# Optimization experiments

Measured on AMD Instinct MI355X. Metric: run time of the kernel, lower is better.

Reference implementation:

```python
import jax, jax.numpy as jnp
import numpy as np

MAX_NODE = 20
SEG = [100, 20, 3200, 160, 400, 20, 400]  # split sizes, total 4300

_DIMS = {"h1": (5, 16), "h2": (16, 8), "h3": (8, 8),
         "f1": (8, 16), "f2": (16, 8), "f3": (8, 8),
         "d1": (13, 16), "d2": (16, 8), "d3": (8, 8),
         "g1": (8, 16), "g2": (16, 8), "g3": (8, 8),
         "fc1": (29, 32), "fc2": (32, 16), "fc3": (16, 8), "fc4": (8, 1)}


def _mk(key, shape):
    return jax.random.normal(key, shape, dtype=jnp.float32) * 0.1


def setup_inputs() -> dict:
    key = jax.random.key(0)
    ks = jax.random.split(key, 8 + 2 * len(_DIMS))
    # assemble the flat [1,4300] input: node feats, masks/adjacency summaries
    ni = jax.random.normal(ks[0], (100,), dtype=jnp.float32)
    valid = jax.random.bernoulli(ks[1], 0.8, (20,)).astype(jnp.float32)
    gmats = jax.random.uniform(ks[2], (3200,), dtype=jnp.float32)
    gmasks = jax.random.bernoulli(ks[3], 0.5, (160,)).astype(jnp.float32)
    summ = jax.random.bernoulli(ks[4], 0.3, (400,)).astype(jnp.float32)
    running = jax.random.bernoulli(ks[5], 0.5, (20,)).astype(jnp.float32)
    backmap = jax.random.bernoulli(ks[6], 0.3, (400,)).astype(jnp.float32)
    inp = jnp.concatenate([ni, valid, gmats, gmasks, summ, running, backmap])[None, :]
    out = {"input": inp}
    i = 8
    for name, (din, dout) in _DIMS.items():
        out[name + "_w"] = _mk(ks[i], (din, dout)); i += 1
        out[name + "_b"] = _mk(ks[i], (dout,)); i += 1
    return out


def reference(input, h1_w, h1_b, h2_w, h2_b, h3_w, h3_b,
              f1_w, f1_b, f2_w, f2_b, f3_w, f3_b,
              d1_w, d1_b, d2_w, d2_b, d3_w, d3_b,
              g1_w, g1_b, g2_w, g2_b, g3_w, g3_b,
              fc1_w, fc1_b, fc2_w, fc2_b, fc3_w, fc3_b, fc4_w, fc4_b):
    relu = jax.nn.relu
    gl = lambda x, w, b: x @ w + b
    x0 = input[0]
    ni = x0[:100].reshape(MAX_NODE, 5)
    valid = x0[100:120].reshape(1, 1, MAX_NODE)
    # x0[120:3320] = gcn_mats (split in original but never used)
    summ = x0[3480:3880].reshape(1, MAX_NODE, MAX_NODE)
    running = x0[3880:3900].reshape(1, 1, MAX_NODE)
    backmap = x0[3900:4300].reshape(1, MAX_NODE, MAX_NODE)
    # original overwrites every gcn_mask with zeros(20,1)
    zmask = jnp.zeros((MAX_NODE, 1), dtype=input.dtype)

    def fblock(y):
        for w, b in ((f1_w, f1_b), (f2_w, f2_b), (f3_w, f3_b),
                     (f1_w, f1_b), (f2_w, f2_b), (f3_w, f3_b)):
            y = relu(gl(y, w, b))
        return y

    x = relu(gl(ni, h1_w, h1_b))
    x = relu(gl(x, h2_w, h2_b))
    x = relu(gl(x, h3_w, h3_b))  # (20, 8)
    y = x
    for blk in range(8):
        src = y if blk == 5 else x  # block 5 forgets to reset y = x (as in source)
        y = fblock(src) * zmask
        x = x + y
    gcn_output = x  # (20, 8)

    xc = jnp.concatenate([ni, gcn_output], axis=1)  # (20, 13)
    s = relu(gl(xc, d1_w, d1_b))
    s = relu(gl(s, d2_w, d2_b))
    s = relu(gl(s, d3_w, d3_b))
    s = jnp.matmul(summ, s)  # (1, 20, 8)
    dag_summary = s
    s = relu(gl(s, g1_w, g1_b))
    s = relu(gl(s, g2_w, g2_b))
    s = relu(gl(s, g3_w, g3_b))
    global_summary = jnp.matmul(running, s)  # (1, 1, 8)
    dag_ext = jnp.matmul(backmap, dag_summary)  # (1, 20, 8)
    glob_ext = jnp.tile(global_summary, (1, MAX_NODE, 1))  # (1, 20, 8)

    merge = jnp.concatenate([ni[None], gcn_output[None], dag_ext, glob_ext], axis=2)  # (1,20,29)
    y2 = relu(gl(merge, fc1_w, fc1_b))
    y2 = relu(gl(y2, fc2_w, fc2_b))
    y2 = relu(gl(y2, fc3_w, fc3_b))
    logits = gl(y2, fc4_w, fc4_b).reshape(1, 1, MAX_NODE)
    logits = logits + (valid - 1.0) * 10000.0
    return jax.nn.softmax(logits, axis=-1).reshape(1, MAX_NODE)
```

## Files before the change

kernel.cpp:

```cpp
#include <hip/hip_runtime.h>
#include <math.h>

#define NT 256

#define CP(dst, src, n) do { for (int i = tid; i < (n); i += NT) (dst)[i] = (src)[i]; } while (0)

template<int DIN, int DOUT, bool RELU>
__device__ __forceinline__ void dense20(int tid, const float* __restrict__ in,
                                        const float* __restrict__ w,
                                        const float* __restrict__ bi,
                                        float* __restrict__ out) {
    constexpr int N = 20 * DOUT;
    #pragma unroll
    for (int i0 = 0; i0 < N; i0 += NT) {
        int i = i0 + tid;
        if (i < N) {
            int r = i / DOUT, c = i % DOUT;
            float acc = bi[c];
            #pragma unroll
            for (int k = 0; k < DIN; ++k)
                acc = fmaf(in[r * DIN + k], w[k * DOUT + c], acc);
            out[i] = RELU ? fmaxf(acc, 0.0f) : acc;
        }
    }
}

__global__ __launch_bounds__(NT)
void fused_net_kernel(const float* __restrict__ inp,
                      const float* __restrict__ h1w, const float* __restrict__ h1b,
                      const float* __restrict__ h2w, const float* __restrict__ h2b,
                      const float* __restrict__ h3w, const float* __restrict__ h3b,
                      const float* __restrict__ d1w, const float* __restrict__ d1b,
                      const float* __restrict__ d2w, const float* __restrict__ d2b,
                      const float* __restrict__ d3w, const float* __restrict__ d3b,
                      const float* __restrict__ g1w, const float* __restrict__ g1b,
                      const float* __restrict__ g2w, const float* __restrict__ g2b,
                      const float* __restrict__ g3w, const float* __restrict__ g3b,
                      const float* __restrict__ fc1w, const float* __restrict__ fc1b,
                      const float* __restrict__ fc2w, const float* __restrict__ fc2b,
                      const float* __restrict__ fc3w, const float* __restrict__ fc3b,
                      const float* __restrict__ fc4w, const float* __restrict__ fc4b,
                      float* __restrict__ out) {
    const int tid = threadIdx.x;

    __shared__ float s_ni[100];
    __shared__ float s_valid[20];
    __shared__ float s_summ[400];
    __shared__ float s_run[20];
    __shared__ float s_back[400];
    __shared__ float s_h1w[80],  s_h1b[16];
    __shared__ float s_h2w[128], s_h2b[8];
    __shared__ float s_h3w[64],  s_h3b[8];
    __shared__ float s_d1w[208], s_d1b[16];
    __shared__ float s_d2w[128], s_d2b[8];
    __shared__ float s_d3w[64],  s_d3b[8];
    __shared__ float s_g1w[128], s_g1b[16];
    __shared__ float s_g2w[128], s_g2b[8];
    __shared__ float s_g3w[64],  s_g3b[8];
    __shared__ float s_fc1w[928], s_fc1b[32];
    __shared__ float s_fc2w[512], s_fc2b[16];
    __shared__ float s_fc3w[128], s_fc3b[8];
    __shared__ float s_fc4w[8],   s_fc4b[1];
    __shared__ float s_bufA[640];
    __shared__ float s_bufB[640];
    __shared__ float s_gcn[160];
    __shared__ float s_dag[160];
    __shared__ float s_glob[8];
    __shared__ float s_logit[20];

    CP(s_ni,    inp,        100);
    CP(s_valid, inp + 100,  20);
    CP(s_summ,  inp + 3480, 400);
    CP(s_run,   inp + 3880, 20);
    CP(s_back,  inp + 3900, 400);
    CP(s_h1w, h1w, 80);   CP(s_h1b, h1b, 16);
    CP(s_h2w, h2w, 128);  CP(s_h2b, h2b, 8);
    CP(s_h3w, h3w, 64);   CP(s_h3b, h3b, 8);
    CP(s_d1w, d1w, 208);  CP(s_d1b, d1b, 16);
    CP(s_d2w, d2w, 128);  CP(s_d2b, d2b, 8);
    CP(s_d3w, d3w, 64);   CP(s_d3b, d3b, 8);
    CP(s_g1w, g1w, 128);  CP(s_g1b, g1b, 16);
    CP(s_g2w, g2w, 128);  CP(s_g2b, g2b, 8);
    CP(s_g3w, g3w, 64);   CP(s_g3b, g3b, 8);
    CP(s_fc1w, fc1w, 928); CP(s_fc1b, fc1b, 32);
    CP(s_fc2w, fc2w, 512); CP(s_fc2b, fc2b, 16);
    CP(s_fc3w, fc3w, 128); CP(s_fc3b, fc3b, 8);
    CP(s_fc4w, fc4w, 8);   CP(s_fc4b, fc4b, 1);
    __syncthreads();

    dense20<5, 16, true>(tid, s_ni,   s_h1w, s_h1b, s_bufA); __syncthreads();
    dense20<16, 8, true>(tid, s_bufA, s_h2w, s_h2b, s_bufB); __syncthreads();
    dense20<8,  8, true>(tid, s_bufB, s_h3w, s_h3b, s_gcn);  __syncthreads();

    {
        int i = tid;
        if (i < 320) {
            int r = i >> 4, c = i & 15;
            float acc = s_d1b[c];
            #pragma unroll
            for (int k = 0; k < 5; ++k)
                acc = fmaf(s_ni[r * 5 + k], s_d1w[k * 16 + c], acc);
            #pragma unroll
            for (int k = 0; k < 8; ++k)
                acc = fmaf(s_gcn[r * 8 + k], s_d1w[(5 + k) * 16 + c], acc);
            s_bufA[i] = fmaxf(acc, 0.0f);
        }
        int j = tid + NT;
        if (j < 320) {
            int r = j >> 4, c = j & 15;
            float acc = s_d1b[c];
            #pragma unroll
            for (int k = 0; k < 5; ++k)
                acc = fmaf(s_ni[r * 5 + k], s_d1w[k * 16 + c], acc);
            #pragma unroll
            for (int k = 0; k < 8; ++k)
                acc = fmaf(s_gcn[r * 8 + k], s_d1w[(5 + k) * 16 + c], acc);
            s_bufA[j] = fmaxf(acc, 0.0f);
        }
    }
    __syncthreads();
    dense20<16, 8, true>(tid, s_bufA, s_d2w, s_d2b, s_bufB); __syncthreads();
    dense20<8,  8, true>(tid, s_bufB, s_d3w, s_d3b, s_bufA); __syncthreads();

    if (tid < 160) {
        int r = tid >> 3, c = tid & 7;
        float acc = 0.0f;
        #pragma unroll
        for (int k = 0; k < 20; ++k)
            acc = fmaf(s_summ[r * 20 + k], s_bufA[k * 8 + c], acc);
        s_dag[tid] = acc;
    }
    __syncthreads();

    dense20<8, 16, true>(tid, s_dag,  s_g1w, s_g1b, s_bufA); __syncthreads();
    dense20<16, 8, true>(tid, s_bufA, s_g2w, s_g2b, s_bufB); __syncthreads();
    dense20<8,  8, true>(tid, s_bufB, s_g3w, s_g3b, s_bufA); __syncthreads();

    if (tid < 160) {
        int r = tid >> 3, c = tid & 7;
        float acc = 0.0f;
        #pragma unroll
        for (int k = 0; k < 20; ++k)
            acc = fmaf(s_back[r * 20 + k], s_dag[k * 8 + c], acc);
        s_bufB[tid] = acc;
    } else if (tid < 168) {
        int c = tid - 160;
        float acc = 0.0f;
        #pragma unroll
        for (int k = 0; k < 20; ++k)
            acc = fmaf(s_run[k], s_bufA[k * 8 + c], acc);
        s_glob[c] = acc;
    }
    __syncthreads();

    #pragma unroll
    for (int i0 = 0; i0 < 640; i0 += NT) {
        int i = i0 + tid;
        if (i < 640) {
            int r = i >> 5, c = i & 31;
            float acc = s_fc1b[c];
            #pragma unroll
            for (int k = 0; k < 5; ++k)
                acc = fmaf(s_ni[r * 5 + k], s_fc1w[k * 32 + c], acc);
            #pragma unroll
            for (int k = 0; k < 8; ++k)
                acc = fmaf(s_gcn[r * 8 + k], s_fc1w[(5 + k) * 32 + c], acc);
            #pragma unroll
            for (int k = 0; k < 8; ++k)
                acc = fmaf(s_bufB[r * 8 + k], s_fc1w[(13 + k) * 32 + c], acc);
            #pragma unroll
            for (int k = 0; k < 8; ++k)
                acc = fmaf(s_glob[k], s_fc1w[(21 + k) * 32 + c], acc);
            s_bufA[i] = fmaxf(acc, 0.0f);
        }
    }
    __syncthreads();
    dense20<32, 16, true>(tid, s_bufA, s_fc2w, s_fc2b, s_bufB); __syncthreads();
    dense20<16, 8, true>(tid, s_bufB, s_fc3w, s_fc3b, s_dag);   __syncthreads();

    if (tid < 20) {
        float acc = s_fc4b[0];
        #pragma unroll
        for (int k = 0; k < 8; ++k)
            acc = fmaf(s_dag[tid * 8 + k], s_fc4w[k], acc);
        s_logit[tid] = acc + (s_valid[tid] - 1.0f) * 10000.0f;
    }
    __syncthreads();

    if (tid == 0) {
        float m = s_logit[0];
        #pragma unroll
        for (int r = 1; r < 20; ++r) m = fmaxf(m, s_logit[r]);
        float e[20];
        float sum = 0.0f;
        #pragma unroll
        for (int r = 0; r < 20; ++r) { e[r] = __expf(s_logit[r] - m); sum += e[r]; }
        float inv = 1.0f / sum;
        #pragma unroll
        for (int r = 0; r < 20; ++r) out[r] = e[r] * inv;
    }
}

extern "C" void kernel_launch(void* const* d_in, const int* in_sizes, int n_in,
                              void* d_out, int out_size, void* d_ws, size_t ws_size,
                              hipStream_t stream) {
    const float* inp = (const float*)d_in[0];
    const float* h1w = (const float*)d_in[1];  const float* h1b = (const float*)d_in[2];
    const float* h2w = (const float*)d_in[3];  const float* h2b = (const float*)d_in[4];
    const float* h3w = (const float*)d_in[5];  const float* h3b = (const float*)d_in[6];
    const float* d1w = (const float*)d_in[13]; const float* d1b = (const float*)d_in[14];
    const float* d2w = (const float*)d_in[15]; const float* d2b = (const float*)d_in[16];
    const float* d3w = (const float*)d_in[17]; const float* d3b = (const float*)d_in[18];
    const float* g1w = (const float*)d_in[19]; const float* g1b = (const float*)d_in[20];
    const float* g2w = (const float*)d_in[21]; const float* g2b = (const float*)d_in[22];
    const float* g3w = (const float*)d_in[23]; const float* g3b = (const float*)d_in[24];
    const float* fc1w = (const float*)d_in[25]; const float* fc1b = (const float*)d_in[26];
    const float* fc2w = (const float*)d_in[27]; const float* fc2b = (const float*)d_in[28];
    const float* fc3w = (const float*)d_in[29]; const float* fc3b = (const float*)d_in[30];
    const float* fc4w = (const float*)d_in[31]; const float* fc4b = (const float*)d_in[32];
    float* out = (float*)d_out;

    fused_net_kernel<<<1, NT, 0, stream>>>(inp,
        h1w, h1b, h2w, h2b, h3w, h3b,
        d1w, d1b, d2w, d2b, d3w, d3b,
        g1w, g1b, g2w, g2b, g3w, g3b,
        fc1w, fc1b, fc2w, fc2b, fc3w, fc3b, fc4w, fc4b,
        out);
}
```

Measured before the change: 125.3 us.

## Shrink block to one wavefront, vectorize shared loads, parallelize softmax output

Reduces the block from 256 to 64 threads, one wave64 wavefront, so barriers become cheap and stages loop over outputs with unrolled strides. Global-to-shared copies use float4 loads with 16-byte-aligned shared arrays. The final softmax is spread across 20 threads that each write one output instead of one thread writing all 20. Each thread now does more serial work per layer, which trades parallel compute for lower synchronisation cost.

```diff
diff --git a/kernel.cpp b/kernel.cpp
--- a/kernel.cpp
+++ b/kernel.cpp
@@ -1,9 +1,11 @@
 #include <hip/hip_runtime.h>
 #include <math.h>
 
-#define NT 256
-
-#define CP(dst, src, n) do { for (int i = tid; i < (n); i += NT) (dst)[i] = (src)[i]; } while (0)
+#define NT 64
+
+#define CP4(dst, src, n) do { \
+    const float4* _s4 = (const float4*)(src); float4* _d4 = (float4*)(dst); \
+    for (int i = tid; i < (n) / 4; i += NT) _d4[i] = _s4[i]; } while (0)
 
 template<int DIN, int DOUT, bool RELU>
 __device__ __forceinline__ void dense20(int tid, const float* __restrict__ in,
@@ -43,92 +45,85 @@
                       float* __restrict__ out) {
     const int tid = threadIdx.x;
 
-    __shared__ float s_ni[100];
-    __shared__ float s_valid[20];
-    __shared__ float s_summ[400];
-    __shared__ float s_run[20];
-    __shared__ float s_back[400];
-    __shared__ float s_h1w[80],  s_h1b[16];
-    __shared__ float s_h2w[128], s_h2b[8];
-    __shared__ float s_h3w[64],  s_h3b[8];
-    __shared__ float s_d1w[208], s_d1b[16];
-    __shared__ float s_d2w[128], s_d2b[8];
-    __shared__ float s_d3w[64],  s_d3b[8];
-    __shared__ float s_g1w[128], s_g1b[16];
-    __shared__ float s_g2w[128], s_g2b[8];
-    __shared__ float s_g3w[64],  s_g3b[8];
-    __shared__ float s_fc1w[928], s_fc1b[32];
-    __shared__ float s_fc2w[512], s_fc2b[16];
-    __shared__ float s_fc3w[128], s_fc3b[8];
-    __shared__ float s_fc4w[8],   s_fc4b[1];
-    __shared__ float s_bufA[640];
-    __shared__ float s_bufB[640];
-    __shared__ float s_gcn[160];
-    __shared__ float s_dag[160];
-    __shared__ float s_glob[8];
-    __shared__ float s_logit[20];
-
-    CP(s_ni,    inp,        100);
-    CP(s_valid, inp + 100,  20);
-    CP(s_summ,  inp + 3480, 400);
-    CP(s_run,   inp + 3880, 20);
-    CP(s_back,  inp + 3900, 400);
-    CP(s_h1w, h1w, 80);   CP(s_h1b, h1b, 16);
-    CP(s_h2w, h2w, 128);  CP(s_h2b, h2b, 8);
-    CP(s_h3w, h3w, 64);   CP(s_h3b, h3b, 8);
-    CP(s_d1w, d1w, 208);  CP(s_d1b, d1b, 16);
-    CP(s_d2w, d2w, 128);  CP(s_d2b, d2b, 8);
-    CP(s_d3w, d3w, 64);   CP(s_d3b, d3b, 8);
-    CP(s_g1w, g1w, 128);  CP(s_g1b, g1b, 16);
-    CP(s_g2w, g2w, 128);  CP(s_g2b, g2b, 8);
-    CP(s_g3w, g3w, 64);   CP(s_g3b, g3b, 8);
-    CP(s_fc1w, fc1w, 928); CP(s_fc1b, fc1b, 32);
-    CP(s_fc2w, fc2w, 512); CP(s_fc2b, fc2b, 16);
-    CP(s_fc3w, fc3w, 128); CP(s_fc3b, fc3b, 8);
-    CP(s_fc4w, fc4w, 8);   CP(s_fc4b, fc4b, 1);
+    __shared__ __align__(16) float s_ni[100];
+    __shared__ __align__(16) float s_valid[20];
+    __shared__ __align__(16) float s_summ[400];
+    __shared__ __align__(16) float s_run[20];
+    __shared__ __align__(16) float s_back[400];
+    __shared__ __align__(16) float s_h1w[80],  s_h1b[16];
+    __shared__ __align__(16) float s_h2w[128], s_h2b[8];
+    __shared__ __align__(16) float s_h3w[64],  s_h3b[8];
+    __shared__ __align__(16) float s_d1w[208], s_d1b[16];
+    __shared__ __align__(16) float s_d2w[128], s_d2b[8];
+    __shared__ __align__(16) float s_d3w[64],  s_d3b[8];
+    __shared__ __align__(16) float s_g1w[128], s_g1b[16];
+    __shared__ __align__(16) float s_g2w[128], s_g2b[8];
+    __shared__ __align__(16) float s_g3w[64],  s_g3b[8];
+    __shared__ __align__(16) float s_fc1w[928], s_fc1b[32];
+    __shared__ __align__(16) float s_fc2w[512], s_fc2b[16];
+    __shared__ __align__(16) float s_fc3w[128], s_fc3b[8];
+    __shared__ __align__(16) float s_fc4w[8];
+    __shared__ float s_fc4b[1];
+    __shared__ __align__(16) float s_bufA[640];
+    __shared__ __align__(16) float s_bufB[640];
+    __shared__ __align__(16) float s_gcn[160];
+    __shared__ __align__(16) float s_dag[160];
+    __shared__ __align__(16) float s_glob[8];
+    __shared__ __align__(16) float s_logit[20];
+
+    CP4(s_ni,    inp,        100);
+    CP4(s_valid, inp + 100,  20);
+    CP4(s_summ,  inp + 3480, 400);
+    CP4(s_run,   inp + 3880, 20);
+    CP4(s_back,  inp + 3900, 400);
+    CP4(s_h1w, h1w, 80);   CP4(s_h1b, h1b, 16);
+    CP4(s_h2w, h2w, 128);  CP4(s_h2b, h2b, 8);
+    CP4(s_h3w, h3w, 64);   CP4(s_h3b, h3b, 8);
+    CP4(s_d1w, d1w, 208);  CP4(s_d1b, d1b, 16);
+    CP4(s_d2w, d2w, 128);  CP4(s_d2b, d2b, 8);
+    CP4(s_d3w, d3w, 64);   CP4(s_d3b, d3b, 8);
+    CP4(s_g1w, g1w, 128);  CP4(s_g1b, g1b, 16);
+    CP4(s_g2w, g2w, 128);  CP4(s_g2b, g2b, 8);
+    CP4(s_g3w, g3w, 64);   CP4(s_g3b, g3b, 8);
+    CP4(s_fc1w, fc1w, 928); CP4(s_fc1b, fc1b, 32);
+    CP4(s_fc2w, fc2w, 512); CP4(s_fc2b, fc2b, 16);
+    CP4(s_fc3w, fc3w, 128); CP4(s_fc3b, fc3b, 8);
+    CP4(s_fc4w, fc4w, 8);
+    if (tid == 0) s_fc4b[0] = fc4b[0];
     __syncthreads();
 
     dense20<5, 16, true>(tid, s_ni,   s_h1w, s_h1b, s_bufA); __syncthreads();
     dense20<16, 8, true>(tid, s_bufA, s_h2w, s_h2b, s_bufB); __syncthreads();
     dense20<8,  8, true>(tid, s_bufB, s_h3w, s_h3b, s_gcn);  __syncthreads();
 
-    {
-        int i = tid;
-        if (i < 320) {
-            int r = i >> 4, c = i & 15;
-            float acc = s_d1b[c];
-            #pragma unroll
-            for (int k = 0; k < 5; ++k)
-                acc = fmaf(s_ni[r * 5 + k], s_d1w[k * 16 + c], acc);
-            #pragma unroll
-            for (int k = 0; k < 8; ++k)
-                acc = fmaf(s_gcn[r * 8 + k], s_d1w[(5 + k) * 16 + c], acc);
-            s_bufA[i] = fmaxf(acc, 0.0f);
-        }
-        int j = tid + NT;
-        if (j < 320) {
-            int r = j >> 4, c = j & 15;
-            float acc = s_d1b[c];
-            #pragma unroll
-            for (int k = 0; k < 5; ++k)
-                acc = fmaf(s_ni[r * 5 + k], s_d1w[k * 16 + c], acc);
-            #pragma unroll
-            for (int k = 0; k < 8; ++k)
-                acc = fmaf(s_gcn[r * 8 + k], s_d1w[(5 + k) * 16 + c], acc);
-            s_bufA[j] = fmaxf(acc, 0.0f);
-        }
+    #pragma unroll
+    for (int i0 = 0; i0 < 320; i0 += NT) {
+        int i = i0 + tid;
+        int r = i >> 4, c = i & 15;
+        float acc = s_d1b[c];
+        #pragma unroll
+        for (int k = 0; k < 5; ++k)
+            acc = fmaf(s_ni[r * 5 + k], s_d1w[k * 16 + c], acc);
+        #pragma unroll
+        for (int k = 0; k < 8; ++k)
+            acc = fmaf(s_gcn[r * 8 + k], s_d1w[(5 + k) * 16 + c], acc);
+        s_bufA[i] = fmaxf(acc, 0.0f);
     }
     __syncthreads();
     dense20<16, 8, true>(tid, s_bufA, s_d2w, s_d2b, s_bufB); __syncthreads();
     dense20<8,  8, true>(tid, s_bufB, s_d3w, s_d3b, s_bufA); __syncthreads();
 
-    if (tid < 160) {
-        int r = tid >> 3, c = tid & 7;
-        float acc = 0.0f;
-        #pragma unroll
-        for (int k = 0; k < 20; ++k)
-            acc = fmaf(s_summ[r * 20 + k], s_bufA[k * 8 + c], acc);
-        s_dag[tid] = acc;
+    #pragma unroll
+    for (int i0 = 0; i0 < 192; i0 += NT) {
+        int i = i0 + tid;
+        if (i < 160) {
+            int r = i >> 3, c = i & 7;
+            float acc = 0.0f;
+            #pragma unroll
+            for (int k = 0; k < 20; ++k)
+                acc = fmaf(s_summ[r * 20 + k], s_bufA[k * 8 + c], acc);
+            s_dag[i] = acc;
+        }
     }
     __syncthreads();
 
@@ -136,43 +131,45 @@
     dense20<16, 8, true>(tid, s_bufA, s_g2w, s_g2b, s_bufB); __syncthreads();
     dense20<8,  8, true>(tid, s_bufB, s_g3w, s_g3b, s_bufA); __syncthreads();
 
-    if (tid < 160) {
-        int r = tid >> 3, c = tid & 7;
-        float acc = 0.0f;
-        #pragma unroll
-        for (int k = 0; k < 20; ++k)
-            acc = fmaf(s_back[r * 20 + k], s_dag[k * 8 + c], acc);
-        s_bufB[tid] = acc;
-    } else if (tid < 168) {
-        int c = tid - 160;
-        float acc = 0.0f;
-        #pragma unroll
-        for (int k = 0; k < 20; ++k)
-            acc = fmaf(s_run[k], s_bufA[k * 8 + c], acc);
-        s_glob[c] = acc;
+    #pragma unroll
+    for (int i0 = 0; i0 < 192; i0 += NT) {
+        int i = i0 + tid;
+        if (i < 160) {
+            int r = i >> 3, c = i & 7;
+            float acc = 0.0f;
+            #pragma unroll
+            for (int k = 0; k < 20; ++k)
+                acc = fmaf(s_back[r * 20 + k], s_dag[k * 8 + c], acc);
+            s_bufB[i] = acc;
+        } else if (i < 168) {
+            int c = i - 160;
+            float acc = 0.0f;
+            #pragma unroll
+            for (int k = 0; k < 20; ++k)
+                acc = fmaf(s_run[k], s_bufA[k * 8 + c], acc);
+            s_glob[c] = acc;
+        }
     }
     __syncthreads();
 
     #pragma unroll
     for (int i0 = 0; i0 < 640; i0 += NT) {
         int i = i0 + tid;
-        if (i < 640) {
-            int r = i >> 5, c = i & 31;
-            float acc = s_fc1b[c];
-            #pragma unroll
-            for (int k = 0; k < 5; ++k)
-                acc = fmaf(s_ni[r * 5 + k], s_fc1w[k * 32 + c], acc);
-            #pragma unroll
-            for (int k = 0; k < 8; ++k)
-                acc = fmaf(s_gcn[r * 8 + k], s_fc1w[(5 + k) * 32 + c], acc);
-            #pragma unroll
-            for (int k = 0; k < 8; ++k)
-                acc = fmaf(s_bufB[r * 8 + k], s_fc1w[(13 + k) * 32 + c], acc);
-            #pragma unroll
-            for (int k = 0; k < 8; ++k)
-                acc = fmaf(s_glob[k], s_fc1w[(21 + k) * 32 + c], acc);
-            s_bufA[i] = fmaxf(acc, 0.0f);
-        }
+        int r = i >> 5, c = i & 31;
+        float acc = s_fc1b[c];
+        #pragma unroll
+        for (int k = 0; k < 5; ++k)
+            acc = fmaf(s_ni[r * 5 + k], s_fc1w[k * 32 + c], acc);
+        #pragma unroll
+        for (int k = 0; k < 8; ++k)
+            acc = fmaf(s_gcn[r * 8 + k], s_fc1w[(5 + k) * 32 + c], acc);
+        #pragma unroll
+        for (int k = 0; k < 8; ++k)
+            acc = fmaf(s_bufB[r * 8 + k], s_fc1w[(13 + k) * 32 + c], acc);
+        #pragma unroll
+        for (int k = 0; k < 8; ++k)
+            acc = fmaf(s_glob[k], s_fc1w[(21 + k) * 32 + c], acc);
+        s_bufA[i] = fmaxf(acc, 0.0f);
     }
     __syncthreads();
     dense20<32, 16, true>(tid, s_bufA, s_fc2w, s_fc2b, s_bufB); __syncthreads();
@@ -187,17 +184,14 @@
     }
     __syncthreads();
 
-    if (tid == 0) {
+    if (tid < 20) {
         float m = s_logit[0];
         #pragma unroll
         for (int r = 1; r < 20; ++r) m = fmaxf(m, s_logit[r]);
-        float e[20];
         float sum = 0.0f;
         #pragma unroll
-        for (int r = 0; r < 20; ++r) { e[r] = __expf(s_logit[r] - m); sum += e[r]; }
-        float inv = 1.0f / sum;
-        #pragma unroll
-        for (int r = 0; r < 20; ++r) out[r] = e[r] * inv;
+        for (int r = 0; r < 20; ++r) sum += __expf(s_logit[r] - m);
+        out[tid] = __expf(s_logit[tid] - m) / sum;
     }
 }
 
```

Measured after the change: 130.1 us. 3.8% more time.
